# Kernel optimization log

Hardware: AMD Instinct MI355X
Metric: run time of the kernel (lower is better)

The kernel has to match this reference:

```python
import jax, jax.numpy as jnp
import numpy as np

POOL, D_MODEL, D_FF, M_DIM = 512, 1024, 4096, 64
B, S, K = 2, 2048, 8


def setup_inputs() -> dict:
    key = jax.random.key(0)
    ks = jax.random.split(key, 8)
    x = jax.random.normal(ks[0], (B, S, D_MODEL), dtype=jnp.float32)
    selected_indices = jax.random.randint(ks[1], (B, S, K), 0, POOL, dtype=jnp.int32)
    pattern_weights = jax.random.normal(ks[2], (B, S, K), dtype=jnp.float32)
    base_patterns = 0.02 * jax.random.normal(ks[3], (POOL, D_FF), dtype=jnp.float32)
    # nn.Linear(d_model, pool_size*mod_dim): weight [P*M, d_model], xavier-uniform
    lim_cm = float(np.sqrt(6.0 / (D_MODEL + POOL * M_DIM)))
    cm_w = jax.random.uniform(ks[4], (POOL * M_DIM, D_MODEL), jnp.float32, -lim_cm, lim_cm)
    cm_b = jnp.zeros((POOL * M_DIM,), jnp.float32)
    adj_proj = 0.01 * jax.random.normal(ks[5], (M_DIM, D_FF), dtype=jnp.float32)
    lim_w2 = float(np.sqrt(6.0 / (D_FF + D_MODEL)))
    w2_w = jax.random.uniform(ks[6], (D_MODEL, D_FF), jnp.float32, -lim_w2, lim_w2)
    w2_b = jnp.zeros((D_MODEL,), jnp.float32)
    return {"x": x, "selected_indices": selected_indices, "pattern_weights": pattern_weights,
            "base_patterns": base_patterns, "cm_w": cm_w, "cm_b": cm_b,
            "adj_proj": adj_proj, "w2_w": w2_w, "w2_b": w2_b}


def reference(x, selected_indices, pattern_weights, base_patterns, cm_w, cm_b, adj_proj, w2_w, w2_b):
    b, s, k = selected_indices.shape
    # gather base firing patterns for selected neurons: [b,s,k,d_ff]
    bp = base_patterns[selected_indices]
    # dense context modulation then gather (matches original module): [b,s,P,M]
    mod = (jnp.einsum('bsd,nd->bsn', x, cm_w) + cm_b).reshape(b, s, POOL, M_DIM)
    sel_mod = jnp.take_along_axis(mod, selected_indices[..., None], axis=2)  # [b,s,k,M]
    adjustments = jnp.einsum('bskm,mf->bskf', sel_mod, adj_proj)
    adjusted = bp + adjustments  # [b,s,k,d_ff]
    w = jax.nn.softmax(pattern_weights, axis=-1)
    combined = jnp.einsum('bsk,bskf->bsf', w, adjusted)  # [b,s,d_ff]
    activated = jax.nn.gelu(combined, approximate=False)  # torch default gelu = exact erf
    return jnp.einsum('bsf,df->bsd', activated, w2_w) + w2_b
```

## Files before the change

### kernel.cpp

```cpp
#include <hip/hip_runtime.h>
#include <math.h>

#define T_    4096
#define K_    8
#define POOL_ 512
#define DM_   1024
#define DFF_  4096
#define MD_   64
#define KC_   576

typedef __bf16 bf16x8 __attribute__((ext_vector_type(8)));
typedef __bf16 bf16x4 __attribute__((ext_vector_type(4)));
typedef float  f32x4  __attribute__((ext_vector_type(4)));

typedef __attribute__((address_space(1))) const void g_void;
typedef __attribute__((address_space(3))) void s_void;

__device__ __forceinline__ void async_ld16(const void* g, void* s) {
    __builtin_amdgcn_global_load_lds((g_void*)g, (s_void*)s, 16, 0, 0);
}
__device__ __forceinline__ float gelu_exact(float g) {
    return 0.5f * g * (1.f + erff(g * 0.70710678118654752f));
}
__device__ __forceinline__ bf16x4 cvt4(float4 v) {
    bf16x4 o;
    o[0] = (__bf16)v.x; o[1] = (__bf16)v.y; o[2] = (__bf16)v.z; o[3] = (__bf16)v.w;
    return o;
}
__device__ __forceinline__ bf16x8 cvt8(float4 a, float4 b) {
    bf16x8 o;
    o[0] = (__bf16)a.x; o[1] = (__bf16)a.y; o[2] = (__bf16)a.z; o[3] = (__bf16)a.w;
    o[4] = (__bf16)b.x; o[5] = (__bf16)b.y; o[6] = (__bf16)b.z; o[7] = (__bf16)b.w;
    return o;
}

__global__ __launch_bounds__(256) void k_hist(const int* __restrict__ sel,
                                              int* __restrict__ counts) {
    int i = blockIdx.x * 256 + threadIdx.x;
    if (i < T_ * K_) atomicAdd(&counts[sel[i]], 1);
}

__global__ __launch_bounds__(512) void k_scan(const int* __restrict__ counts,
                                              int* __restrict__ offsets,
                                              int* __restrict__ cursor) {
    __shared__ int s[512];
    const int t = threadIdx.x;
    const int c = counts[t];
    s[t] = c;
    __syncthreads();
    for (int d = 1; d < 512; d <<= 1) {
        int v = (t >= d) ? s[t - d] : 0;
        __syncthreads();
        s[t] += v;
        __syncthreads();
    }
    offsets[t] = s[t] - c;
    cursor[t]  = s[t] - c;
    if (t == 511) offsets[512] = s[511];
}

__global__ __launch_bounds__(256) void k_scatter(const int* __restrict__ sel,
                                                 int* __restrict__ cursor,
                                                 int* __restrict__ bucket,
                                                 int* __restrict__ rank) {
    int i = blockIdx.x * 256 + threadIdx.x;
    if (i < T_ * K_) {
        int p = sel[i];
        int pos = atomicAdd(&cursor[p], 1);
        bucket[pos] = i;
        rank[i] = pos;
    }
}

__global__ __launch_bounds__(256) void k_cvt(const float* __restrict__ src,
                                             __bf16* __restrict__ dst, int n16) {
    int i = blockIdx.x * 256 + threadIdx.x;
    if (i >= n16) return;
    const float4* s = (const float4*)src + (long)i * 4;
    float4 a = s[0], b = s[1], c = s[2], d = s[3];
    bf16x8 o0 = cvt8(a, b), o1 = cvt8(c, d);
    bf16x8* dp = (bf16x8*)dst + (long)i * 2;
    dp[0] = o0; dp[1] = o1;
}

__global__ __launch_bounds__(256) void k_selmod(
    const __bf16* __restrict__ xb, const float* __restrict__ cm_w,
    const int* __restrict__ bucket, const int* __restrict__ offsets,
    float* __restrict__ Y0, float* __restrict__ Y1,
    float* __restrict__ Y2, float* __restrict__ Y3)
{
    const int p   = blockIdx.x;
    const int kh  = blockIdx.y;
    const int off = offsets[p];
    int n = offsets[p + 1] - off;
    if (n <= 0) return;
    if (n > 256) n = 256;
    float* Y = (kh == 0) ? Y0 : (kh == 1) ? Y1 : (kh == 2) ? Y2 : Y3;

    const int tid  = threadIdx.x;
    const int wave = tid >> 6, lane = tid & 63;
    const int quad = lane >> 4, l15 = lane & 15;

    __shared__ int list[256];
    __shared__ __align__(16) __bf16 Wl[64][264];

    {
        const int wr = tid >> 6;
        const int wc = (tid & 63) * 4;
        const float* wsrc = cm_w + (long)(p * 64 + wr) * DM_ + kh * 256 + wc;
        float4 wv[16];
        #pragma unroll
        for (int j = 0; j < 16; ++j)
            wv[j] = *(const float4*)(wsrc + (long)j * 4 * DM_);
        #pragma unroll
        for (int j = 0; j < 16; ++j)
            *(bf16x4*)&Wl[wr + j * 4][wc] = cvt4(wv[j]);
    }
    for (int i = tid; i < n; i += 256) list[i] = bucket[off + i] >> 3;
    __syncthreads();

    const int nch = (n + 15) >> 4;
    for (int c = wave; c < nch; c += 4) {
        int row = c * 16 + l15; if (row >= n) row = n - 1;
        const __bf16* xrow = xb + (long)list[row] * DM_ + kh * 256 + quad * 8;

        f32x4 a0 = {}, a1 = {}, a2 = {}, a3 = {};
        #pragma unroll
        for (int ks = 0; ks < 8; ++ks) {
            const bf16x8 afr = *(const bf16x8*)(xrow + ks * 32);
            const bf16x8 b0 = *(const bf16x8*)&Wl[ 0 + l15][ks * 32 + quad * 8];
            const bf16x8 b1 = *(const bf16x8*)&Wl[16 + l15][ks * 32 + quad * 8];
            const bf16x8 b2 = *(const bf16x8*)&Wl[32 + l15][ks * 32 + quad * 8];
            const bf16x8 b3 = *(const bf16x8*)&Wl[48 + l15][ks * 32 + quad * 8];
            a0 = __builtin_amdgcn_mfma_f32_16x16x32_bf16(afr, b0, a0, 0, 0, 0);
            a1 = __builtin_amdgcn_mfma_f32_16x16x32_bf16(afr, b1, a1, 0, 0, 0);
            a2 = __builtin_amdgcn_mfma_f32_16x16x32_bf16(afr, b2, a2, 0, 0, 0);
            a3 = __builtin_amdgcn_mfma_f32_16x16x32_bf16(afr, b3, a3, 0, 0, 0);
        }
        #pragma unroll
        for (int r = 0; r < 4; ++r) {
            const int prow = c * 16 + quad * 4 + r;
            if (prow < n) {
                float* yr = Y + (long)(off + prow) * MD_ + l15;
                yr[ 0] = a0[r];
                yr[16] = a1[r];
                yr[32] = a2[r];
                yr[48] = a3[r];
            }
        }
    }
}

__global__ __launch_bounds__(256) void k_wdense(
    const float* __restrict__ Y0, const float* __restrict__ Y1,
    const float* __restrict__ Y2, const float* __restrict__ Y3,
    const int* __restrict__ sel, const int* __restrict__ rank,
    const float* __restrict__ pw, const float* __restrict__ cm_b,
    __bf16* __restrict__ Wd)
{
    const int tid = threadIdx.x;
    const int tt = tid >> 6, m = tid & 63;
    const int t = blockIdx.x * 4 + tt;
    __shared__ float w_s[4][8];
    __shared__ int   sidx[4][8];
    __shared__ int   rnk[4][8];
    __shared__ __align__(16) __bf16 row[4][KC_];

    if (m < 8) {
        w_s[tt][m]  = pw[t * 8 + m];
        sidx[tt][m] = sel[t * 8 + m];
        rnk[tt][m]  = rank[t * 8 + m];
    }
    __syncthreads();
    if (m == 0) {
        float mx = w_s[tt][0];
        #pragma unroll
        for (int k = 1; k < 8; ++k) mx = fmaxf(mx, w_s[tt][k]);
        float sum = 0.f;
        #pragma unroll
        for (int k = 0; k < 8; ++k) { float e = expf(w_s[tt][k] - mx); w_s[tt][k] = e; sum += e; }
        float inv = 1.f / sum;
        #pragma unroll
        for (int k = 0; k < 8; ++k) w_s[tt][k] *= inv;
    }
    __syncthreads();
    *(uint4*)&row[tt][m * 8] = make_uint4(0, 0, 0, 0);
    {
        float a = 0.f;
        #pragma unroll
        for (int k = 0; k < 8; ++k) {
            const long yb = (long)rnk[tt][k] * MD_ + m;
            float y = cm_b[sidx[tt][k] * 64 + m] + Y0[yb] + Y1[yb] + Y2[yb] + Y3[yb];
            a += w_s[tt][k] * y;
        }
        row[tt][512 + m] = (__bf16)a;
    }
    __syncthreads();
    if (m == 0) {
        #pragma unroll
        for (int k = 0; k < 8; ++k) {
            int c = sidx[tt][k];
            row[tt][c] = (__bf16)((float)row[tt][c] + w_s[tt][k]);
        }
    }
    __syncthreads();
    const uint4* src = (const uint4*)&row[0][0];
    uint4* dst = (uint4*)(Wd + (long)blockIdx.x * 4 * KC_);
    for (int e = tid; e < 4 * KC_ * 2 / 16; e += 256) dst[e] = src[e];
}

__global__ __launch_bounds__(256) void k_buildP(
    const float* __restrict__ bp, const float* __restrict__ adj,
    __bf16* __restrict__ P)
{
    __shared__ __bf16 tile[64][72];
    const int tid = threadIdx.x;
    const int bx = blockIdx.x, f0 = blockIdx.y * 64;
    const float* src = (bx < 8) ? (bp + (long)bx * 64 * DFF_) : adj;
    for (int e = tid; e < 4096; e += 256) {
        int f = e & 63, c = e >> 6;
        tile[c][f] = (__bf16)src[(long)c * DFF_ + f0 + f];
    }
    __syncthreads();
    const int c0 = bx * 64;
    for (int e = tid; e < 4096; e += 256) {
        int c = e & 63, f = e >> 6;
        P[(long)(f0 + f) * KC_ + c0 + c] = tile[c][f];
    }
}

__global__ __launch_bounds__(256) void k_actgemm(
    const __bf16* __restrict__ A, const __bf16* __restrict__ Bw,
    __bf16* __restrict__ act)
{
    __shared__ __align__(16) __bf16 sA[128 * 32];
    __shared__ __align__(16) __bf16 sB[128 * 32];
    const int tid  = threadIdx.x;
    const int tm   = blockIdx.y * 128, tn = blockIdx.x * 128;
    const int wave = tid >> 6, lane = tid & 63, quad = lane >> 4, l15 = lane & 15;
    const int wm   = (wave >> 1) * 64, wn = (wave & 1) * 64;

    f32x4 acc[4][4] = {};

    const int e    = tid * 8;
    const int srow = e >> 5;
    const int scol = e & 31;
    const __bf16* agp0 = A  + ((long)(tm + srow)      * KC_ + scol);
    const __bf16* agp1 = A  + ((long)(tm + 64 + srow) * KC_ + scol);
    const __bf16* bgp0 = Bw + ((long)(tn + srow)      * KC_ + scol);
    const __bf16* bgp1 = Bw + ((long)(tn + 64 + srow) * KC_ + scol);
    void* sa0 = (void*)(sA + e);
    void* sa1 = (void*)(sA + 2048 + e);
    void* sb0 = (void*)(sB + e);
    void* sb1 = (void*)(sB + 2048 + e);

    for (int kk = 0; kk < KC_; kk += 32) {
        async_ld16(agp0 + kk, sa0);
        async_ld16(agp1 + kk, sa1);
        async_ld16(bgp0 + kk, sb0);
        async_ld16(bgp1 + kk, sb1);
        __syncthreads();
        bf16x8 af[4], bf[4];
        #pragma unroll
        for (int i = 0; i < 4; ++i)
            af[i] = *(const bf16x8*)(sA + (wm + i * 16 + l15) * 32 + quad * 8);
        #pragma unroll
        for (int j = 0; j < 4; ++j)
            bf[j] = *(const bf16x8*)(sB + (wn + j * 16 + l15) * 32 + quad * 8);
        #pragma unroll
        for (int i = 0; i < 4; ++i)
            #pragma unroll
            for (int j = 0; j < 4; ++j)
                acc[i][j] = __builtin_amdgcn_mfma_f32_16x16x32_bf16(af[i], bf[j], acc[i][j], 0, 0, 0);
        __syncthreads();
    }

    #pragma unroll
    for (int j = 0; j < 4; ++j) {
        const int col = tn + wn + j * 16 + l15;
        #pragma unroll
        for (int i = 0; i < 4; ++i) {
            const int row = tm + wm + i * 16 + quad * 4;
            #pragma unroll
            for (int r = 0; r < 4; ++r)
                act[(long)(row + r) * DFF_ + col] = (__bf16)gelu_exact(acc[i][j][r]);
        }
    }
}

__global__ __launch_bounds__(256) void k_outgemm(
    const __bf16* __restrict__ A, const __bf16* __restrict__ Bw,
    const float* __restrict__ bias, float* __restrict__ out)
{
    __shared__ __align__(16) __bf16 sA[128 * 128];
    __shared__ __align__(16) __bf16 sB[128 * 128];
    const int tid  = threadIdx.x;
    const int tm   = blockIdx.y * 128, tn = blockIdx.x * 128;
    const int wave = tid >> 6, lane = tid & 63, quad = lane >> 4, l15 = lane & 15;
    const int wm   = (wave >> 1) * 64, wn = (wave & 1) * 64;

    f32x4 acc[4][4] = {};

    const int e  = tid * 8;
    const int r0 = e >> 5;
    const int cc = e & 31;

    for (int kk = 0; kk < DFF_; kk += 128) {
        #pragma unroll
        for (int s = 0; s < 4; ++s) {
            #pragma unroll
            for (int q = 0; q < 2; ++q) {
                async_ld16(A  + (long)(tm + q * 64 + r0) * DFF_ + kk + s * 32 + cc,
                           (void*)(sA + s * 4096 + q * 2048 + e));
                async_ld16(Bw + (long)(tn + q * 64 + r0) * DFF_ + kk + s * 32 + cc,
                           (void*)(sB + s * 4096 + q * 2048 + e));
            }
        }
        __syncthreads();
        #pragma unroll
        for (int s = 0; s < 4; ++s) {
            bf16x8 af[4], bf[4];
            #pragma unroll
            for (int i = 0; i < 4; ++i)
                af[i] = *(const bf16x8*)(sA + s * 4096 + (wm + i * 16 + l15) * 32 + quad * 8);
            #pragma unroll
            for (int j = 0; j < 4; ++j)
                bf[j] = *(const bf16x8*)(sB + s * 4096 + (wn + j * 16 + l15) * 32 + quad * 8);
            #pragma unroll
            for (int i = 0; i < 4; ++i)
                #pragma unroll
                for (int j = 0; j < 4; ++j)
                    acc[i][j] = __builtin_amdgcn_mfma_f32_16x16x32_bf16(af[i], bf[j], acc[i][j], 0, 0, 0);
        }
        __syncthreads();
    }

    #pragma unroll
    for (int j = 0; j < 4; ++j) {
        const int col = tn + wn + j * 16 + l15;
        const float bj = bias[col];
        #pragma unroll
        for (int i = 0; i < 4; ++i) {
            const int row = tm + wm + i * 16 + quad * 4;
            #pragma unroll
            for (int r = 0; r < 4; ++r)
                out[(long)(row + r) * 1024 + col] = acc[i][j][r] + bj;
        }
    }
}

extern "C" void kernel_launch(void* const* d_in, const int* in_sizes, int n_in,
                              void* d_out, int out_size, void* d_ws, size_t ws_size,
                              hipStream_t stream) {
    const float* x    = (const float*)d_in[0];
    const int*   sel  = (const int*)  d_in[1];
    const float* pw   = (const float*)d_in[2];
    const float* bp   = (const float*)d_in[3];
    const float* cm_w = (const float*)d_in[4];
    const float* cm_b = (const float*)d_in[5];
    const float* adj  = (const float*)d_in[6];
    const float* w2   = (const float*)d_in[7];
    const float* w2b  = (const float*)d_in[8];
    float* out = (float*)d_out;

    char* ws = (char*)d_ws;
    __bf16* x_bf = (__bf16*)ws;
    __bf16* act  = (__bf16*)ws;
    float*  Yp1  = (float*)(ws + (size_t) 8 * 1024 * 1024);
    float*  Yp2  = (float*)(ws + (size_t)16 * 1024 * 1024);
    float*  Yp3  = (float*)(ws + (size_t)24 * 1024 * 1024);
    __bf16* P    = (__bf16*)(ws + (size_t)32 * 1024 * 1024);
    __bf16* w2bf = (__bf16*)(ws + (size_t)37 * 1024 * 1024);
    char*  bins  = ws + (size_t)45 * 1024 * 1024;
    int* bucket  = (int*)bins;
    int* rank    = (int*)(bins + 131072);
    int* counts  = (int*)(bins + 262144);
    int* cursor  = (int*)(bins + 264192);
    int* offsets = (int*)(bins + 266240);

    float*  Yp0 = (float*)d_out;
    __bf16* Wd  = (__bf16*)((char*)d_out + (size_t)8 * 1024 * 1024);

    hipMemsetAsync(counts, 0, 4096, stream);
    k_hist   <<<128, 256, 0, stream>>>(sel, counts);
    k_scan   <<<1,   512, 0, stream>>>(counts, offsets, cursor);
    k_scatter<<<128, 256, 0, stream>>>(sel, cursor, bucket, rank);
    k_cvt    <<<1024, 256, 0, stream>>>(x, x_bf, T_ * DM_ / 16);
    k_selmod <<<dim3(POOL_, 4), 256, 0, stream>>>(x_bf, cm_w, bucket, offsets,
                                                  Yp0, Yp1, Yp2, Yp3);
    k_wdense <<<T_ / 4, 256, 0, stream>>>(Yp0, Yp1, Yp2, Yp3, sel, rank, pw, cm_b, Wd);
    k_buildP <<<dim3(9, 64), 256, 0, stream>>>(bp, adj, P);
    k_cvt    <<<1024, 256, 0, stream>>>(w2, w2bf, DM_ * DFF_ / 16);
    k_actgemm<<<dim3(DFF_ / 128, T_ / 128), 256, 0, stream>>>(Wd, P, act);
    k_outgemm<<<dim3(DM_ / 128, T_ / 128), 256, 0, stream>>>(act, w2bf, w2b, out);
}
```

Measured before the change: 400.8 us.

## Double-buffer LDS tiles in activation and output GEMMs to overlap loads with MFMA

```diff
diff --git a/kernel.cpp b/kernel.cpp
--- a/kernel.cpp
+++ b/kernel.cpp
@@ -104,6 +104,9 @@
     __shared__ int list[256];
     __shared__ __align__(16) __bf16 Wl[64][264];
 
+    int lv = -1;
+    if (tid < n) lv = bucket[off + tid] >> 3;
+
     {
         const int wr = tid >> 6;
         const int wc = (tid & 63) * 4;
@@ -116,7 +119,7 @@
         for (int j = 0; j < 16; ++j)
             *(bf16x4*)&Wl[wr + j * 4][wc] = cvt4(wv[j]);
     }
-    for (int i = tid; i < n; i += 256) list[i] = bucket[off + i] >> 3;
+    if (tid < n) list[tid] = lv;
     __syncthreads();
 
     const int nch = (n + 15) >> 4;
@@ -233,8 +236,8 @@
     const __bf16* __restrict__ A, const __bf16* __restrict__ Bw,
     __bf16* __restrict__ act)
 {
-    __shared__ __align__(16) __bf16 sA[128 * 32];
-    __shared__ __align__(16) __bf16 sB[128 * 32];
+    __shared__ __align__(16) __bf16 sA[2 * 128 * 32];
+    __shared__ __align__(16) __bf16 sB[2 * 128 * 32];
     const int tid  = threadIdx.x;
     const int tm   = blockIdx.y * 128, tn = blockIdx.x * 128;
     const int wave = tid >> 6, lane = tid & 63, quad = lane >> 4, l15 = lane & 15;
@@ -249,30 +252,40 @@
     const __bf16* agp1 = A  + ((long)(tm + 64 + srow) * KC_ + scol);
     const __bf16* bgp0 = Bw + ((long)(tn + srow)      * KC_ + scol);
     const __bf16* bgp1 = Bw + ((long)(tn + 64 + srow) * KC_ + scol);
-    void* sa0 = (void*)(sA + e);
-    void* sa1 = (void*)(sA + 2048 + e);
-    void* sb0 = (void*)(sB + e);
-    void* sb1 = (void*)(sB + 2048 + e);
-
-    for (int kk = 0; kk < KC_; kk += 32) {
-        async_ld16(agp0 + kk, sa0);
-        async_ld16(agp1 + kk, sa1);
-        async_ld16(bgp0 + kk, sb0);
-        async_ld16(bgp1 + kk, sb1);
-        __syncthreads();
+
+    const int NT = KC_ / 32;
+
+    async_ld16(agp0, (void*)(sA + e));
+    async_ld16(agp1, (void*)(sA + 2048 + e));
+    async_ld16(bgp0, (void*)(sB + e));
+    async_ld16(bgp1, (void*)(sB + 2048 + e));
+    __syncthreads();
+
+    int cur = 0;
+    for (int t = 0; t < NT; ++t) {
+        if (t + 1 < NT) {
+            const int kk = (t + 1) * 32;
+            const int nb = (cur ^ 1) * 4096;
+            async_ld16(agp0 + kk, (void*)(sA + nb + e));
+            async_ld16(agp1 + kk, (void*)(sA + nb + 2048 + e));
+            async_ld16(bgp0 + kk, (void*)(sB + nb + e));
+            async_ld16(bgp1 + kk, (void*)(sB + nb + 2048 + e));
+        }
+        const int cb = cur * 4096;
         bf16x8 af[4], bf[4];
         #pragma unroll
         for (int i = 0; i < 4; ++i)
-            af[i] = *(const bf16x8*)(sA + (wm + i * 16 + l15) * 32 + quad * 8);
+            af[i] = *(const bf16x8*)(sA + cb + (wm + i * 16 + l15) * 32 + quad * 8);
         #pragma unroll
         for (int j = 0; j < 4; ++j)
-            bf[j] = *(const bf16x8*)(sB + (wn + j * 16 + l15) * 32 + quad * 8);
+            bf[j] = *(const bf16x8*)(sB + cb + (wn + j * 16 + l15) * 32 + quad * 8);
         #pragma unroll
         for (int i = 0; i < 4; ++i)
             #pragma unroll
             for (int j = 0; j < 4; ++j)
                 acc[i][j] = __builtin_amdgcn_mfma_f32_16x16x32_bf16(af[i], bf[j], acc[i][j], 0, 0, 0);
         __syncthreads();
+        cur ^= 1;
     }
 
     #pragma unroll
@@ -292,8 +305,8 @@
     const __bf16* __restrict__ A, const __bf16* __restrict__ Bw,
     const float* __restrict__ bias, float* __restrict__ out)
 {
-    __shared__ __align__(16) __bf16 sA[128 * 128];
-    __shared__ __align__(16) __bf16 sB[128 * 128];
+    __shared__ __align__(16) __bf16 sA[2 * 2 * 128 * 32];
+    __shared__ __align__(16) __bf16 sB[2 * 2 * 128 * 32];
     const int tid  = threadIdx.x;
     const int tm   = blockIdx.y * 128, tn = blockIdx.x * 128;
     const int wave = tid >> 6, lane = tid & 63, quad = lane >> 4, l15 = lane & 15;
@@ -305,27 +318,44 @@
     const int r0 = e >> 5;
     const int cc = e & 31;
 
-    for (int kk = 0; kk < DFF_; kk += 128) {
-        #pragma unroll
-        for (int s = 0; s < 4; ++s) {
-            #pragma unroll
-            for (int q = 0; q < 2; ++q) {
-                async_ld16(A  + (long)(tm + q * 64 + r0) * DFF_ + kk + s * 32 + cc,
-                           (void*)(sA + s * 4096 + q * 2048 + e));
-                async_ld16(Bw + (long)(tn + q * 64 + r0) * DFF_ + kk + s * 32 + cc,
-                           (void*)(sB + s * 4096 + q * 2048 + e));
-            }
-        }
-        __syncthreads();
-        #pragma unroll
-        for (int s = 0; s < 4; ++s) {
+    const int NT = DFF_ / 64;
+
+    #pragma unroll
+    for (int s = 0; s < 2; ++s)
+        #pragma unroll
+        for (int q = 0; q < 2; ++q) {
+            async_ld16(A  + (long)(tm + q * 64 + r0) * DFF_ + s * 32 + cc,
+                       (void*)(sA + s * 4096 + q * 2048 + e));
+            async_ld16(Bw + (long)(tn + q * 64 + r0) * DFF_ + s * 32 + cc,
+                       (void*)(sB + s * 4096 + q * 2048 + e));
+        }
+    __syncthreads();
+
+    int cur = 0;
+    for (int t = 0; t < NT; ++t) {
+        if (t + 1 < NT) {
+            const int kk = (t + 1) * 64;
+            const int nb = (cur ^ 1) * 8192;
+            #pragma unroll
+            for (int s = 0; s < 2; ++s)
+                #pragma unroll
+                for (int q = 0; q < 2; ++q) {
+                    async_ld16(A  + (long)(tm + q * 64 + r0) * DFF_ + kk + s * 32 + cc,
+                               (void*)(sA + nb + s * 4096 + q * 2048 + e));
+                    async_ld16(Bw + (long)(tn + q * 64 + r0) * DFF_ + kk + s * 32 + cc,
+                               (void*)(sB + nb + s * 4096 + q * 2048 + e));
+                }
+        }
+        const int cb = cur * 8192;
+        #pragma unroll
+        for (int s = 0; s < 2; ++s) {
             bf16x8 af[4], bf[4];
             #pragma unroll
             for (int i = 0; i < 4; ++i)
-                af[i] = *(const bf16x8*)(sA + s * 4096 + (wm + i * 16 + l15) * 32 + quad * 8);
+                af[i] = *(const bf16x8*)(sA + cb + s * 4096 + (wm + i * 16 + l15) * 32 + quad * 8);
             #pragma unroll
             for (int j = 0; j < 4; ++j)
-                bf[j] = *(const bf16x8*)(sB + s * 4096 + (wn + j * 16 + l15) * 32 + quad * 8);
+                bf[j] = *(const bf16x8*)(sB + cb + s * 4096 + (wn + j * 16 + l15) * 32 + quad * 8);
             #pragma unroll
             for (int i = 0; i < 4; ++i)
                 #pragma unroll
@@ -333,6 +363,7 @@
                     acc[i][j] = __builtin_amdgcn_mfma_f32_16x16x32_bf16(af[i], bf[j], acc[i][j], 0, 0, 0);
         }
         __syncthreads();
+        cur ^= 1;
     }
 
     #pragma unroll
```

Measured after the change: 415.3 us. +3.6%, slower.

## Double-buffer output GEMM LDS loads and shrink tile to 64x128

Applied to the files above, without the earlier changes.

```diff
diff --git a/kernel.cpp b/kernel.cpp
--- a/kernel.cpp
+++ b/kernel.cpp
@@ -292,47 +292,66 @@
     const __bf16* __restrict__ A, const __bf16* __restrict__ Bw,
     const float* __restrict__ bias, float* __restrict__ out)
 {
-    __shared__ __align__(16) __bf16 sA[128 * 128];
-    __shared__ __align__(16) __bf16 sB[128 * 128];
+    __shared__ __align__(16) __bf16 sA[2 * 2 * 64 * 32];
+    __shared__ __align__(16) __bf16 sB[2 * 2 * 128 * 32];
     const int tid  = threadIdx.x;
-    const int tm   = blockIdx.y * 128, tn = blockIdx.x * 128;
+    const int tm   = blockIdx.y * 64, tn = blockIdx.x * 128;
     const int wave = tid >> 6, lane = tid & 63, quad = lane >> 4, l15 = lane & 15;
-    const int wm   = (wave >> 1) * 64, wn = (wave & 1) * 64;
-
-    f32x4 acc[4][4] = {};
+    const int wm   = (wave >> 1) * 32, wn = (wave & 1) * 64;
+
+    f32x4 acc[2][4] = {};
 
     const int e  = tid * 8;
     const int r0 = e >> 5;
     const int cc = e & 31;
 
-    for (int kk = 0; kk < DFF_; kk += 128) {
-        #pragma unroll
-        for (int s = 0; s < 4; ++s) {
-            #pragma unroll
-            for (int q = 0; q < 2; ++q) {
-                async_ld16(A  + (long)(tm + q * 64 + r0) * DFF_ + kk + s * 32 + cc,
-                           (void*)(sA + s * 4096 + q * 2048 + e));
-                async_ld16(Bw + (long)(tn + q * 64 + r0) * DFF_ + kk + s * 32 + cc,
-                           (void*)(sB + s * 4096 + q * 2048 + e));
+    const int NT = DFF_ / 64;
+
+    #pragma unroll
+    for (int s = 0; s < 2; ++s) {
+        async_ld16(A + (long)(tm + r0) * DFF_ + s * 32 + cc,
+                   (void*)(sA + s * 2048 + e));
+        #pragma unroll
+        for (int q = 0; q < 2; ++q)
+            async_ld16(Bw + (long)(tn + q * 64 + r0) * DFF_ + s * 32 + cc,
+                       (void*)(sB + s * 4096 + q * 2048 + e));
+    }
+    __syncthreads();
+
+    int cur = 0;
+    for (int t = 0; t < NT; ++t) {
+        if (t + 1 < NT) {
+            const int kk = (t + 1) * 64;
+            const int na = (cur ^ 1) * 4096;
+            const int nb = (cur ^ 1) * 8192;
+            #pragma unroll
+            for (int s = 0; s < 2; ++s) {
+                async_ld16(A + (long)(tm + r0) * DFF_ + kk + s * 32 + cc,
+                           (void*)(sA + na + s * 2048 + e));
+                #pragma unroll
+                for (int q = 0; q < 2; ++q)
+                    async_ld16(Bw + (long)(tn + q * 64 + r0) * DFF_ + kk + s * 32 + cc,
+                               (void*)(sB + nb + s * 4096 + q * 2048 + e));
             }
         }
-        __syncthreads();
-        #pragma unroll
-        for (int s = 0; s < 4; ++s) {
-            bf16x8 af[4], bf[4];
-            #pragma unroll
-            for (int i = 0; i < 4; ++i)
-                af[i] = *(const bf16x8*)(sA + s * 4096 + (wm + i * 16 + l15) * 32 + quad * 8);
+        const int ca = cur * 4096, cb = cur * 8192;
+        #pragma unroll
+        for (int s = 0; s < 2; ++s) {
+            bf16x8 af[2], bf[4];
+            #pragma unroll
+            for (int i = 0; i < 2; ++i)
+                af[i] = *(const bf16x8*)(sA + ca + s * 2048 + (wm + i * 16 + l15) * 32 + quad * 8);
             #pragma unroll
             for (int j = 0; j < 4; ++j)
-                bf[j] = *(const bf16x8*)(sB + s * 4096 + (wn + j * 16 + l15) * 32 + quad * 8);
-            #pragma unroll
-            for (int i = 0; i < 4; ++i)
+                bf[j] = *(const bf16x8*)(sB + cb + s * 4096 + (wn + j * 16 + l15) * 32 + quad * 8);
+            #pragma unroll
+            for (int i = 0; i < 2; ++i)
                 #pragma unroll
                 for (int j = 0; j < 4; ++j)
                     acc[i][j] = __builtin_amdgcn_mfma_f32_16x16x32_bf16(af[i], bf[j], acc[i][j], 0, 0, 0);
         }
         __syncthreads();
+        cur ^= 1;
     }
 
     #pragma unroll
@@ -340,7 +359,7 @@
         const int col = tn + wn + j * 16 + l15;
         const float bj = bias[col];
         #pragma unroll
-        for (int i = 0; i < 4; ++i) {
+        for (int i = 0; i < 2; ++i) {
             const int row = tm + wm + i * 16 + quad * 4;
             #pragma unroll
             for (int r = 0; r < 4; ++r)
@@ -392,5 +411,5 @@
     k_buildP <<<dim3(9, 64), 256, 0, stream>>>(bp, adj, P);
     k_cvt    <<<1024, 256, 0, stream>>>(w2, w2bf, DM_ * DFF_ / 16);
     k_actgemm<<<dim3(DFF_ / 128, T_ / 128), 256, 0, stream>>>(Wd, P, act);
-    k_outgemm<<<dim3(DM_ / 128, T_ / 128), 256, 0, stream>>>(act, w2bf, w2b, out);
-}
+    k_outgemm<<<dim3(DM_ / 128, T_ / 64), 256, 0, stream>>>(act, w2bf, w2b, out);
+}
```

Result: no change. 398.8 us (-0.5%).
